# Kernel tuning notes

Measured on AMD Instinct MI355X. Metric: run time of the kernel, lower is better.

The kernel has to match this reference:

```python
import jax, jax.numpy as jnp
import numpy as np

H = 56; W = 56; WS = 7; SS = 3; NH = 12; DIM = 384; B = 32
N = WS * WS                      # 49 tokens per window
NW = (H // WS) * (W // WS)       # 64 windows per image
HID = 4 * DIM
EPS = 1e-5


def _rel_index():
    coords = np.stack(np.meshgrid(np.arange(WS), np.arange(WS), indexing='ij'))  # [2,ws,ws]
    cf = coords.reshape(2, -1)
    rel = (cf[:, :, None] - cf[:, None, :]).transpose(1, 2, 0)  # [N,N,2]
    rel[..., 0] += WS - 1
    rel[..., 1] += WS - 1
    rel[..., 0] *= 2 * WS - 1
    return rel.sum(-1).astype(np.int32)  # [N,N] in [0,169)


def _attn_mask():
    img = np.zeros((H, W), np.float32)
    cnt = 0
    sl = (slice(0, -WS), slice(-WS, -SS), slice(-SS, None))
    for h in sl:
        for w in sl:
            img[h, w] = cnt
            cnt += 1
    mw = img.reshape(H // WS, WS, W // WS, WS).transpose(0, 2, 1, 3).reshape(-1, N)  # [nW,N]
    am = mw[:, None, :] - mw[:, :, None]  # [nW,N,N]
    return np.where(am != 0, np.float32(-100.0), np.float32(0.0)).astype(np.float32)


def _ln(x, g, b):
    m = jnp.mean(x, axis=-1, keepdims=True)
    v = jnp.mean(jnp.square(x - m), axis=-1, keepdims=True)
    return (x - m) * jax.lax.rsqrt(v + EPS) * g + b


def setup_inputs() -> dict:
    key = jax.random.key(0)
    ks = jax.random.split(key, 8)
    s = 0.02
    return {
        'x': jax.random.normal(ks[0], (B, H * W, DIM), jnp.float32),
        'qkv_w': jax.random.normal(ks[1], (3 * DIM, DIM), jnp.float32) * s,
        'qkv_b': jnp.zeros((3 * DIM,), jnp.float32),
        'proj_w': jax.random.normal(ks[2], (DIM, DIM), jnp.float32) * s,
        'proj_b': jnp.zeros((DIM,), jnp.float32),
        'rpb_table': jax.random.normal(ks[3], ((2 * WS - 1) ** 2, NH), jnp.float32) * s,
        'ln1_g': jnp.ones((DIM,), jnp.float32),
        'ln1_b': jnp.zeros((DIM,), jnp.float32),
        'fc1_w': jax.random.normal(ks[4], (HID, DIM), jnp.float32) * s,
        'fc1_b': jnp.zeros((HID,), jnp.float32),
        'fc2_w': jax.random.normal(ks[5], (DIM, HID), jnp.float32) * s,
        'fc2_b': jnp.zeros((DIM,), jnp.float32),
        'ln2_g': jnp.ones((DIM,), jnp.float32),
        'ln2_b': jnp.zeros((DIM,), jnp.float32),
        'attn_mask': jnp.asarray(_attn_mask()),
        'rel_idx': jnp.asarray(_rel_index()),
    }


def reference(x, qkv_w, qkv_b, proj_w, proj_b, rpb_table, ln1_g, ln1_b,
              fc1_w, fc1_b, fc2_w, fc2_b, ln2_g, ln2_b, attn_mask, rel_idx):
    Bb, L, C = x.shape
    hd = C // NH
    scale = hd ** -0.5
    shortcut = x
    # cyclic shift
    xs = jnp.roll(x.reshape(Bb, H, W, C), (-SS, -SS), axis=(1, 2))
    # window partition -> [Bb*nW, N, C]
    xw = xs.reshape(Bb, H // WS, WS, W // WS, WS, C).transpose(0, 1, 3, 2, 4, 5).reshape(-1, N, C)
    # qkv
    qkv = (xw @ qkv_w.T + qkv_b).reshape(-1, N, 3, NH, hd).transpose(2, 0, 3, 1, 4)
    q, k, v = qkv[0] * scale, qkv[1], qkv[2]          # [Bb*nW, NH, N, hd]
    attn = jnp.einsum('whnd,whmd->whnm', q, k)        # [Bb*nW, NH, N, N]
    bias = rpb_table[rel_idx.reshape(-1)].reshape(N, N, NH).transpose(2, 0, 1)
    attn = attn + bias[None]
    # shifted-window mask
    attn = attn.reshape(Bb, NW, NH, N, N) + attn_mask[None, :, None]
    attn = jax.nn.softmax(attn.reshape(-1, NH, N, N), axis=-1)
    out = jnp.einsum('whnm,whmd->whnd', attn, v).transpose(0, 2, 1, 3).reshape(-1, N, C)
    out = out @ proj_w.T + proj_b
    # window reverse + roll back
    xs = out.reshape(Bb, H // WS, W // WS, WS, WS, C).transpose(0, 1, 3, 2, 4, 5).reshape(Bb, H, W, C)
    xs = jnp.roll(xs, (SS, SS), axis=(1, 2)).reshape(Bb, L, C)
    # post-norm residuals (as in source: shortcut + norm(attn_out); x += norm(ffn(x)))
    x1 = shortcut + _ln(xs, ln1_g, ln1_b)
    y = jax.nn.gelu(x1 @ fc1_w.T + fc1_b, approximate=False) @ fc2_w.T + fc2_b
    return x1 + _ln(y, ln2_g, ln2_b)
```

## Files before the change

kernel.cpp:

```cpp
#include <hip/hip_runtime.h>
#include <hip/hip_bf16.h>
#include <math.h>

typedef __hip_bfloat16 bf16;
typedef __bf16 bf16x8 __attribute__((ext_vector_type(8)));
typedef float f32x4 __attribute__((ext_vector_type(4)));

#define HH 56
#define WW 56
#define WSZ 7
#define SSH 3
#define NHEAD 12
#define CDIM 384
#define BBATCH 32
#define NTOK 49
#define NWIN 64
#define HIDD 1536
#define HD 32
#define NWTOT (BBATCH*NWIN)
#define MROWS (NWTOT*NTOK)
#define MHALF (MROWS/2)
#define LTOT (HH*WW)
#define EPSLN 1e-5f
#define QSCALE 0.17677669529663687f
#define NEGBIG -1e30f

enum { M_QK = 0, M_V = 1, M_FC1 = 2 };

__device__ __forceinline__ void gload16(const void* g, void* l) {
    __builtin_amdgcn_global_load_lds(
        (const __attribute__((address_space(1))) void*)g,
        (__attribute__((address_space(3))) void*)l, 16, 0, 0);
}

__device__ __forceinline__ unsigned short bfbits(float v) {
    bf16 b = __float2bfloat16(v);
    return *reinterpret_cast<unsigned short*>(&b);
}

__device__ __forceinline__ float fast_gelu(float v) {
    return v / (1.0f + __expf(-1.59576912f * v * fmaf(0.044715f, v * v, 1.0f)));
}

__device__ __forceinline__ int xcd_swz(int orig, int nwg) {
    const int q = nwg >> 3, r = nwg & 7;
    const int xcd = orig & 7, loc = orig >> 3;
    return (xcd < r ? xcd * (q + 1) : r * (q + 1) + (xcd - r) * q) + loc;
}

__global__ __launch_bounds__(256) void cvt_k(const float* __restrict__ src,
                                             bf16* __restrict__ dst, int n) {
    int i = blockIdx.x * 256 + threadIdx.x;
    if (i < n) dst[i] = __float2bfloat16(src[i]);
}

__global__ __launch_bounds__(256)
void tbl_k(const float* __restrict__ rpb, const int* __restrict__ relidx,
           const float* __restrict__ amask, float* __restrict__ tbl) {
    int idx = blockIdx.x * 256 + threadIdx.x;
    int m = idx & 63, n = (idx >> 6) & 63;
    int h = (idx >> 12) % NHEAD, wi = idx / (64 * 64 * NHEAD);
    float v;
    if (m >= NTOK) v = NEGBIG;
    else if (n >= NTOK) v = 0.f;
    else v = rpb[relidx[n * NTOK + m] * NHEAD + h] + amask[((long)wi * NTOK + n) * NTOK + m];
    tbl[idx] = v;
}

__global__ __launch_bounds__(256) void gather_k(const float* __restrict__ x,
                                                bf16* __restrict__ xw, int rbase) {
    int idx = blockIdx.x * 256 + threadIdx.x;
    int rr_l = idx / 96, c4 = (idx % 96) * 4;
    int rr = rbase + rr_l;
    int w = rr / 49, ti = rr % 49;
    int b = w >> 6, wi = w & 63;
    int hy = (wi >> 3) * 7 + ti / 7;
    int hx = (wi & 7) * 7 + ti % 7;
    int sh = hy + SSH; if (sh >= HH) sh -= HH;
    int sw = hx + SSH; if (sw >= WW) sw -= WW;
    float4 v = *(const float4*)&x[((long)b * LTOT + sh * WW + sw) * CDIM + c4];
    ushort4 u = { bfbits(v.x), bfbits(v.y), bfbits(v.z), bfbits(v.w) };
    *(ushort4*)&xw[(long)rr_l * CDIM + c4] = u;
}

template<int MODE, int KDIM, int NTN>
__global__ __launch_bounds__(256, 4)
void mgemm_k(const bf16* __restrict__ A, const bf16* __restrict__ Wt,
             const float* __restrict__ bias, void* __restrict__ Outp)
{
    constexpr bool SWAP = (MODE != M_V);
    __shared__ bf16 As[2][128 * 32];
    __shared__ bf16 Bs[2][128 * 32];
    const int tid = threadIdx.x;
    const int wid = tid >> 6, lane = tid & 63;

    const int gid = xcd_swz(blockIdx.x, gridDim.x);
    const int m0 = (gid / NTN) * 128;
    const int n0 = (gid % NTN) * 128;

    const int strow = lane >> 2, stseg = lane & 3;
    const int swseg = stseg ^ ((strow >> 1) & 3);
    const bf16* Ag = A + (long)(m0 + wid * 32 + strow) * KDIM + swseg * 8;
    const bf16* Wg = Wt + (long)(n0 + wid * 32 + strow) * KDIM + swseg * 8;

    const int wr = (wid >> 1) * 64, wc = (wid & 1) * 64;
    const int l15 = lane & 15, g4 = lane >> 4;
    const int sa = g4 ^ ((l15 >> 1) & 3);

    f32x4 acc[4][4] = {};

    auto STAGE = [&](int b, int t) {
#pragma unroll
        for (int i = 0; i < 2; ++i)
            gload16(Ag + (long)(i * 16) * KDIM + t * 32, &As[b][(wid * 32 + i * 16) * 32]);
#pragma unroll
        for (int i = 0; i < 2; ++i)
            gload16(Wg + (long)(i * 16) * KDIM + t * 32, &Bs[b][(wid * 32 + i * 16) * 32]);
    };

    const int nt = KDIM / 32;
    STAGE(0, 0);
    STAGE(1, 1);
    asm volatile("s_waitcnt vmcnt(4)" ::: "memory");
    __builtin_amdgcn_s_barrier();

    int buf = 0;
    for (int t = 0; t < nt; ++t) {
        bf16x8 af[4], bfr[4];
#pragma unroll
        for (int i = 0; i < 4; ++i) {
            af[i]  = *(const bf16x8*)&As[buf][(wr + i * 16 + l15) * 32 + sa * 8];
            bfr[i] = *(const bf16x8*)&Bs[buf][(wc + i * 16 + l15) * 32 + sa * 8];
        }
        __builtin_amdgcn_sched_barrier(0);
        asm volatile("s_waitcnt lgkmcnt(0)" ::: "memory");
        __builtin_amdgcn_sched_barrier(0);
        __builtin_amdgcn_s_barrier();
        if (t + 2 < nt) STAGE(buf, t + 2);
#pragma unroll
        for (int mi = 0; mi < 4; ++mi)
#pragma unroll
            for (int ni = 0; ni < 4; ++ni) {
                if (SWAP)
                    acc[ni][mi] = __builtin_amdgcn_mfma_f32_16x16x32_bf16(
                        bfr[ni], af[mi], acc[ni][mi], 0, 0, 0);
                else
                    acc[mi][ni] = __builtin_amdgcn_mfma_f32_16x16x32_bf16(
                        af[mi], bfr[ni], acc[mi][ni], 0, 0, 0);
            }
        if (t + 2 < nt) { asm volatile("s_waitcnt vmcnt(4)" ::: "memory"); }
        else            { asm volatile("s_waitcnt vmcnt(0)" ::: "memory"); }
        __builtin_amdgcn_s_barrier();
        buf ^= 1;
    }

    if (MODE == M_V) {
#pragma unroll
        for (int mi = 0; mi < 4; ++mi) {
            const int mb = m0 + wr + mi * 16 + g4 * 4;
            const int wv_ = mb / 49, ti0 = mb - wv_ * 49;
#pragma unroll
            for (int ni = 0; ni < 4; ++ni) {
                const int n = n0 + wc + ni * 16 + l15;
                const int h = n >> 5, d = n & 31;
                const float bn = bias[n];
                float v4[4];
#pragma unroll
                for (int j = 0; j < 4; ++j) v4[j] = acc[mi][ni][j] + bn;
                if (ti0 <= 45) {
                    ushort4 u = { bfbits(v4[0]), bfbits(v4[1]), bfbits(v4[2]), bfbits(v4[3]) };
                    *(ushort4*)&((bf16*)Outp)[(((long)wv_ * NHEAD + h) * HD + d) * 64 + ti0] = u;
                } else {
#pragma unroll
                    for (int j = 0; j < 4; ++j) {
                        const int m = mb + j;
                        const int w2 = m / 49, ti = m - w2 * 49;
                        ((bf16*)Outp)[(((long)w2 * NHEAD + h) * HD + d) * 64 + ti]
                            = __float2bfloat16(v4[j]);
                    }
                }
            }
        }
    } else {
        long rowbase[4];
        int wq_[4], ti_[4];
#pragma unroll
        for (int mi = 0; mi < 4; ++mi) {
            const int m = m0 + wr + mi * 16 + l15;
            if (MODE == M_QK) { wq_[mi] = m / 49; ti_[mi] = m - wq_[mi] * 49; }
            else              { rowbase[mi] = (long)m * HIDD; }
        }
#pragma unroll
        for (int ni = 0; ni < 4; ++ni) {
            const int nb = n0 + wc + ni * 16 + g4 * 4;
            const float4 bn = *(const float4*)&bias[nb];
            const float bb[4] = { bn.x, bn.y, bn.z, bn.w };
#pragma unroll
            for (int mi = 0; mi < 4; ++mi) {
                float v4[4];
#pragma unroll
                for (int j = 0; j < 4; ++j) v4[j] = acc[ni][mi][j] + bb[j];
                if (MODE == M_FC1) {
#pragma unroll
                    for (int j = 0; j < 4; ++j) v4[j] = fast_gelu(v4[j]);
                } else if (MODE == M_QK) {
                    if (nb < CDIM) {
#pragma unroll
                        for (int j = 0; j < 4; ++j) v4[j] *= QSCALE;
                    }
                }
                ushort4 u = { bfbits(v4[0]), bfbits(v4[1]), bfbits(v4[2]), bfbits(v4[3]) };
                if (MODE == M_QK) {
                    const int which = nb >= CDIM;
                    const int hb = (nb - which * CDIM) >> 5, d0 = nb & 31;
                    *(ushort4*)&((bf16*)Outp)[
                        ((((long)wq_[mi] * 2 + which) * NHEAD + hb) * NTOK + ti_[mi]) * HD + d0] = u;
                } else {
                    *(ushort4*)&((bf16*)Outp)[rowbase[mi] + nb] = u;
                }
            }
        }
    }
}

template<int KDIM, bool SCATTER>
__global__ __launch_bounds__(256, 2)
void gemm_ln_k(const bf16* __restrict__ A, const bf16* __restrict__ Wt,
               const float* __restrict__ bias, const bf16* __restrict__ resid,
               const float* __restrict__ lng, const float* __restrict__ lnb,
               float* __restrict__ outf, bf16* __restrict__ outb, int mbase)
{
    __shared__ bf16 As[2][64 * 32];
    __shared__ bf16 Bs[2][384 * 32];
    __shared__ float lnp[512];
    const int tid = threadIdx.x;
    const int wid = tid >> 6, lane = tid & 63;

    const int m0 = xcd_swz(blockIdx.x, gridDim.x) * 64;

    const int strow = tid >> 2, stseg = tid & 3;
    const int swr = stseg ^ ((strow >> 1) & 3);
    const bf16* Ag = A + (long)(m0 + strow) * KDIM + swr * 8;
    const bf16* Wg = Wt + (long)strow * KDIM + swr * 8;

    const int wc = wid * 96;
    const int l15 = lane & 15, g4 = lane >> 4;
    const int sa = g4 ^ ((l15 >> 1) & 3);

    f32x4 acc[6][4] = {};

    auto STAGE = [&](int b, int t) {
        gload16(Ag + t * 32, &As[b][strow * 32 + stseg * 8]);
#pragma unroll
        for (int i = 0; i < 6; ++i)
            gload16(Wg + (long)(i * 64) * KDIM + t * 32,
                    &Bs[b][(strow + i * 64) * 32 + stseg * 8]);
    };

    const int nt = KDIM / 32;
    STAGE(0, 0);
    STAGE(1, 1);
    asm volatile("s_waitcnt vmcnt(7)" ::: "memory");
    __builtin_amdgcn_s_barrier();

    int buf = 0;
    for (int t = 0; t < nt; ++t) {
        bf16x8 af[4], bfr[6];
#pragma unroll
        for (int i = 0; i < 4; ++i)
            af[i] = *(const bf16x8*)&As[buf][(i * 16 + l15) * 32 + sa * 8];
#pragma unroll
        for (int i = 0; i < 6; ++i)
            bfr[i] = *(const bf16x8*)&Bs[buf][(wc + i * 16 + l15) * 32 + sa * 8];
        __builtin_amdgcn_sched_barrier(0);
        asm volatile("s_waitcnt lgkmcnt(0)" ::: "memory");
        __builtin_amdgcn_sched_barrier(0);
        __builtin_amdgcn_s_barrier();
        if (t + 2 < nt) STAGE(buf, t + 2);
#pragma unroll
        for (int ni = 0; ni < 6; ++ni)
#pragma unroll
            for (int mi = 0; mi < 4; ++mi)
                acc[ni][mi] = __builtin_amdgcn_mfma_f32_16x16x32_bf16(
                    bfr[ni], af[mi], acc[ni][mi], 0, 0, 0);
        if (t + 2 < nt) { asm volatile("s_waitcnt vmcnt(7)" ::: "memory"); }
        else            { asm volatile("s_waitcnt vmcnt(0)" ::: "memory"); }
        __builtin_amdgcn_s_barrier();
        buf ^= 1;
    }

    float psum[4] = {}, psq[4] = {};
#pragma unroll
    for (int ni = 0; ni < 6; ++ni) {
        const int nb = wc + ni * 16 + g4 * 4;
        const float4 bn = *(const float4*)&bias[nb];
        const float bb[4] = { bn.x, bn.y, bn.z, bn.w };
#pragma unroll
        for (int mi = 0; mi < 4; ++mi)
#pragma unroll
            for (int j = 0; j < 4; ++j) {
                float v = acc[ni][mi][j] + bb[j];
                acc[ni][mi][j] = v;
                psum[mi] += v; psq[mi] += v * v;
            }
    }
#pragma unroll
    for (int mi = 0; mi < 4; ++mi) {
        psum[mi] += __shfl_xor(psum[mi], 16); psum[mi] += __shfl_xor(psum[mi], 32);
        psq[mi]  += __shfl_xor(psq[mi], 16);  psq[mi]  += __shfl_xor(psq[mi], 32);
    }
    if (g4 == 0) {
#pragma unroll
        for (int mi = 0; mi < 4; ++mi) {
            const int r = mi * 16 + l15;
            lnp[wid * 64 + r] = psum[mi];
            lnp[256 + wid * 64 + r] = psq[mi];
        }
    }
    __syncthreads();

#pragma unroll
    for (int mi = 0; mi < 4; ++mi) {
        const int r = mi * 16 + l15;
        const float s  = lnp[r] + lnp[64 + r] + lnp[128 + r] + lnp[192 + r];
        const float sq = lnp[256 + r] + lnp[320 + r] + lnp[384 + r] + lnp[448 + r];
        const float mean = s * (1.f / 384.f);
        const float rstd = rsqrtf(sq * (1.f / 384.f) - mean * mean + EPSLN);

        const long rl = m0 + r;
        long dst;
        if (SCATTER) {
            const int m = mbase + (int)rl;
            int w = m / 49, ti = m - w * 49;
            int b = w >> 6, wi = w & 63;
            int hy = (wi >> 3) * 7 + ti / 7;
            int hx = (wi & 7) * 7 + ti % 7;
            int dh = hy + SSH; if (dh >= HH) dh -= HH;
            int dw = hx + SSH; if (dw >= WW) dw -= WW;
            dst = (long)b * LTOT + dh * WW + dw - mbase;
        } else {
            dst = mbase + rl;
        }
#pragma unroll
        for (int ni = 0; ni < 6; ++ni) {
            const int c = wc + ni * 16 + g4 * 4;
            const float4 gv = *(const float4*)&lng[c];
            const float4 bv = *(const float4*)&lnb[c];
            ushort4 xv = *(const ushort4*)&resid[rl * CDIM + c];
            float x0 = __bfloat162float(*(bf16*)&xv.x);
            float x1 = __bfloat162float(*(bf16*)&xv.y);
            float x2 = __bfloat162float(*(bf16*)&xv.z);
            float x3 = __bfloat162float(*(bf16*)&xv.w);
            float r0 = x0 + (acc[ni][mi][0] - mean) * rstd * gv.x + bv.x;
            float r1 = x1 + (acc[ni][mi][1] - mean) * rstd * gv.y + bv.y;
            float r2 = x2 + (acc[ni][mi][2] - mean) * rstd * gv.z + bv.z;
            float r3 = x3 + (acc[ni][mi][3] - mean) * rstd * gv.w + bv.w;
            if (SCATTER) {
                ushort4 u = { bfbits(r0), bfbits(r1), bfbits(r2), bfbits(r3) };
                *(ushort4*)&outb[dst * CDIM + c] = u;
            } else {
                float4 o = { r0, r1, r2, r3 };
                *(float4*)&outf[dst * CDIM + c] = o;
            }
        }
    }
}

__global__ __launch_bounds__(256)
void mattn_k(const bf16* __restrict__ qk, const bf16* __restrict__ vT,
             const float* __restrict__ tbl, bf16* __restrict__ attn_out)
{
    __shared__ bf16 Plds[4][64 * 72];
    const int tid = threadIdx.x, wid = tid >> 6, lane = tid & 63;
    const int t = blockIdx.x * 4 + wid;
    const int w = t / NHEAD, h = t % NHEAD, wi = w & 63;
    const int l15 = lane & 15, g = lane >> 4;
    const bf16* qb = qk + ((long)(w * 2 + 0) * NHEAD + h) * (NTOK * HD);
    const bf16* kb = qk + ((long)(w * 2 + 1) * NHEAD + h) * (NTOK * HD);
    const bf16* vt = vT + ((long)w * NHEAD + h) * (HD * 64);
    const float* Tb = tbl + (long)(wi * NHEAD + h) * 64 * 64;
    char* Pw = (char*)&Plds[wid][0];

    bf16x8 kf[4], qf[4];
#pragma unroll
    for (int i = 0; i < 4; ++i) {
        kf[i] = *(const bf16x8*)&kb[(16 * i + l15) * HD + 8 * g];
        qf[i] = *(const bf16x8*)&qb[(16 * i + l15) * HD + 8 * g];
    }
    f32x4 s[4][4] = {};
#pragma unroll
    for (int mi = 0; mi < 4; ++mi)
#pragma unroll
        for (int ni = 0; ni < 4; ++ni)
            s[mi][ni] = __builtin_amdgcn_mfma_f32_16x16x32_bf16(
                kf[mi], qf[ni], s[mi][ni], 0, 0, 0);

#pragma unroll
    for (int ni = 0; ni < 4; ++ni) {
        const int n = 16 * ni + l15;
#pragma unroll
        for (int mi = 0; mi < 4; ++mi) {
            float4 tv = *(const float4*)&Tb[(long)n * 64 + 16 * mi + 4 * g];
            s[mi][ni][0] += tv.x; s[mi][ni][1] += tv.y;
            s[mi][ni][2] += tv.z; s[mi][ni][3] += tv.w;
        }
        float mx = NEGBIG;
#pragma unroll
        for (int mi = 0; mi < 4; ++mi)
#pragma unroll
            for (int j = 0; j < 4; ++j) mx = fmaxf(mx, s[mi][ni][j]);
        mx = fmaxf(mx, __shfl_xor(mx, 16));
        mx = fmaxf(mx, __shfl_xor(mx, 32));
        float sum = 0.f;
#pragma unroll
        for (int mi = 0; mi < 4; ++mi)
#pragma unroll
            for (int j = 0; j < 4; ++j) {
                float e = expf(s[mi][ni][j] - mx);
                s[mi][ni][j] = e; sum += e;
            }
        sum += __shfl_xor(sum, 16);
        sum += __shfl_xor(sum, 32);
        const float r = 1.0f / sum;
#pragma unroll
        for (int mi = 0; mi < 4; ++mi) {
            ushort4 u;
            u.x = bfbits(s[mi][ni][0] * r);
            u.y = bfbits(s[mi][ni][1] * r);
            u.z = bfbits(s[mi][ni][2] * r);
            u.w = bfbits(s[mi][ni][3] * r);
            *(ushort4*)(Pw + (long)n * 144 + (16 * mi + 4 * g) * 2) = u;
        }
    }

    f32x4 o[4][2] = {};
#pragma unroll
    for (int kk = 0; kk < 2; ++kk) {
        bf16x8 vf[2];
        vf[0] = *(const bf16x8*)&vt[(long)(l15) * 64 + 32 * kk + 8 * g];
        vf[1] = *(const bf16x8*)&vt[(long)(16 + l15) * 64 + 32 * kk + 8 * g];
#pragma unroll
        for (int rt = 0; rt < 4; ++rt) {
            bf16x8 pf = *(const bf16x8*)(Pw + (long)(16 * rt + l15) * 144 + (32 * kk + 8 * g) * 2);
            o[rt][0] = __builtin_amdgcn_mfma_f32_16x16x32_bf16(pf, vf[0], o[rt][0], 0, 0, 0);
            o[rt][1] = __builtin_amdgcn_mfma_f32_16x16x32_bf16(pf, vf[1], o[rt][1], 0, 0, 0);
        }
    }

#pragma unroll
    for (int rt = 0; rt < 4; ++rt)
#pragma unroll
        for (int dt = 0; dt < 2; ++dt)
#pragma unroll
            for (int j = 0; j < 4; ++j) {
                int n = 16 * rt + 4 * g + j;
                if (n < NTOK)
                    attn_out[((long)w * NTOK + n) * CDIM + h * HD + 16 * dt + l15]
                        = __float2bfloat16(o[rt][dt][j]);
            }
}

extern "C" void kernel_launch(void* const* d_in, const int* in_sizes, int n_in,
                              void* d_out, int out_size, void* d_ws, size_t ws_size,
                              hipStream_t stream)
{
    const float* x      = (const float*)d_in[0];
    const float* qkv_w  = (const float*)d_in[1];
    const float* qkv_b  = (const float*)d_in[2];
    const float* proj_w = (const float*)d_in[3];
    const float* proj_b = (const float*)d_in[4];
    const float* rpb    = (const float*)d_in[5];
    const float* ln1_g  = (const float*)d_in[6];
    const float* ln1_b  = (const float*)d_in[7];
    const float* fc1_w  = (const float*)d_in[8];
    const float* fc1_b  = (const float*)d_in[9];
    const float* fc2_w  = (const float*)d_in[10];
    const float* fc2_b  = (const float*)d_in[11];
    const float* ln2_g  = (const float*)d_in[12];
    const float* ln2_b  = (const float*)d_in[13];
    const float* amask  = (const float*)d_in[14];
    const int*   relidx = (const int*)d_in[15];
    float* out = (float*)d_out;
    char*  ws  = (char*)d_ws;

    bf16*  wq    = (bf16*) (ws + 0L);
    bf16*  wp    = (bf16*) (ws + 884736L);
    bf16*  w1    = (bf16*) (ws + 1179648L);
    bf16*  w2    = (bf16*) (ws + 2359296L);
    float* tbl   = (float*)(ws + 3538944L);
    bf16*  xw_h  = (bf16*) (ws + 16121856L);
    bf16*  qkb_h = (bf16*) (ws + 54657024L);
    bf16*  vT_h  = (bf16*) (ws + 131727360L);
    bf16*  att_h = (bf16*) (ws + 182059008L);
    bf16*  x1b_h = (bf16*) (ws + 220594176L);
    bf16*  H1_h  = (bf16*) (ws + 16121856L);

    dim3 b256(256);

    cvt_k<<<dim3((3*CDIM*CDIM + 255)/256), b256, 0, stream>>>(qkv_w, wq, 3*CDIM*CDIM);
    cvt_k<<<dim3((CDIM*CDIM + 255)/256), b256, 0, stream>>>(proj_w, wp, CDIM*CDIM);
    cvt_k<<<dim3((HIDD*CDIM + 255)/256), b256, 0, stream>>>(fc1_w, w1, HIDD*CDIM);
    cvt_k<<<dim3((CDIM*HIDD + 255)/256), b256, 0, stream>>>(fc2_w, w2, CDIM*HIDD);
    tbl_k<<<dim3(64*12*64*64/256), b256, 0, stream>>>(rpb, relidx, amask, tbl);

    for (int c = 0; c < 2; ++c) {
        const int mb = c * MHALF;
        gather_k<<<dim3(MHALF * 96 / 256), b256, 0, stream>>>(x, xw_h, mb);
        mgemm_k<M_QK, CDIM, 6><<<dim3((MHALF/128)*6), b256, 0, stream>>>(
            xw_h, wq, qkv_b, (void*)qkb_h);
        mgemm_k<M_V, CDIM, 3><<<dim3((MHALF/128)*3), b256, 0, stream>>>(
            xw_h, wq + (long)2*CDIM*CDIM, qkv_b + 2*CDIM, (void*)vT_h);
        mattn_k<<<dim3(1024 * NHEAD / 4), b256, 0, stream>>>(qkb_h, vT_h, tbl, att_h);
        gemm_ln_k<CDIM, true><<<dim3(MHALF/64), b256, 0, stream>>>(
            att_h, wp, proj_b, xw_h, ln1_g, ln1_b, nullptr, x1b_h, mb);
        mgemm_k<M_FC1, CDIM, 12><<<dim3((MHALF/128)*12), b256, 0, stream>>>(
            x1b_h, w1, fc1_b, (void*)H1_h);
        gemm_ln_k<HIDD, false><<<dim3(MHALF/64), b256, 0, stream>>>(
            H1_h, w2, fc2_b, x1b_h, ln2_g, ln2_b, out, nullptr, mb);
    }
}
```

Before: 888.4 us.

## Enlarge GEMM+LayerNorm tile to 128 rows with 512-thread blocks

The fused GEMM+LayerNorm kernels now process 128 rows per block using 8 waves arranged 2x4, instead of 64 rows with 4 waves. Each staged 384-column weight tile is therefore reused across twice as many rows, which halves weight traffic from global memory and L2 per output row. The per-thread load count in the staging pipeline and the LN partial-sum buffer are adjusted to match. The trade-off is larger LDS use per block, half as many blocks, and a launch bound of 4 blocks of 512 threads that may constrain registers.

```diff
diff --git a/kernel.cpp b/kernel.cpp
--- a/kernel.cpp
+++ b/kernel.cpp
@@ -224,26 +224,27 @@
 }
 
 template<int KDIM, bool SCATTER>
-__global__ __launch_bounds__(256, 2)
+__global__ __launch_bounds__(512, 4)
 void gemm_ln_k(const bf16* __restrict__ A, const bf16* __restrict__ Wt,
                const float* __restrict__ bias, const bf16* __restrict__ resid,
                const float* __restrict__ lng, const float* __restrict__ lnb,
                float* __restrict__ outf, bf16* __restrict__ outb, int mbase)
 {
-    __shared__ bf16 As[2][64 * 32];
+    __shared__ bf16 As[2][128 * 32];
     __shared__ bf16 Bs[2][384 * 32];
-    __shared__ float lnp[512];
+    __shared__ float lnp[1024];
     const int tid = threadIdx.x;
     const int wid = tid >> 6, lane = tid & 63;
 
-    const int m0 = xcd_swz(blockIdx.x, gridDim.x) * 64;
+    const int m0 = xcd_swz(blockIdx.x, gridDim.x) * 128;
 
     const int strow = tid >> 2, stseg = tid & 3;
-    const int swr = stseg ^ ((strow >> 1) & 3);
-    const bf16* Ag = A + (long)(m0 + strow) * KDIM + swr * 8;
-    const bf16* Wg = Wt + (long)strow * KDIM + swr * 8;
-
-    const int wc = wid * 96;
+    const int sws = stseg ^ ((strow >> 1) & 3);
+    const bf16* Ag = A + (long)(m0 + strow) * KDIM + sws * 8;
+    const bf16* Wg = Wt + (long)strow * KDIM + sws * 8;
+
+    const int wm = wid >> 2, wn = wid & 3;
+    const int wr = wm * 64, wc = wn * 96;
     const int l15 = lane & 15, g4 = lane >> 4;
     const int sa = g4 ^ ((l15 >> 1) & 3);
 
@@ -252,15 +253,15 @@
     auto STAGE = [&](int b, int t) {
         gload16(Ag + t * 32, &As[b][strow * 32 + stseg * 8]);
 #pragma unroll
-        for (int i = 0; i < 6; ++i)
-            gload16(Wg + (long)(i * 64) * KDIM + t * 32,
-                    &Bs[b][(strow + i * 64) * 32 + stseg * 8]);
+        for (int p = 0; p < 3; ++p)
+            gload16(Wg + (long)(p * 128) * KDIM + t * 32,
+                    &Bs[b][(p * 128 + strow) * 32 + stseg * 8]);
     };
 
     const int nt = KDIM / 32;
     STAGE(0, 0);
     STAGE(1, 1);
-    asm volatile("s_waitcnt vmcnt(7)" ::: "memory");
+    asm volatile("s_waitcnt vmcnt(4)" ::: "memory");
     __builtin_amdgcn_s_barrier();
 
     int buf = 0;
@@ -268,7 +269,7 @@
         bf16x8 af[4], bfr[6];
 #pragma unroll
         for (int i = 0; i < 4; ++i)
-            af[i] = *(const bf16x8*)&As[buf][(i * 16 + l15) * 32 + sa * 8];
+            af[i] = *(const bf16x8*)&As[buf][(wr + i * 16 + l15) * 32 + sa * 8];
 #pragma unroll
         for (int i = 0; i < 6; ++i)
             bfr[i] = *(const bf16x8*)&Bs[buf][(wc + i * 16 + l15) * 32 + sa * 8];
@@ -283,7 +284,7 @@
             for (int mi = 0; mi < 4; ++mi)
                 acc[ni][mi] = __builtin_amdgcn_mfma_f32_16x16x32_bf16(
                     bfr[ni], af[mi], acc[ni][mi], 0, 0, 0);
-        if (t + 2 < nt) { asm volatile("s_waitcnt vmcnt(7)" ::: "memory"); }
+        if (t + 2 < nt) { asm volatile("s_waitcnt vmcnt(4)" ::: "memory"); }
         else            { asm volatile("s_waitcnt vmcnt(0)" ::: "memory"); }
         __builtin_amdgcn_s_barrier();
         buf ^= 1;
@@ -312,18 +313,18 @@
     if (g4 == 0) {
 #pragma unroll
         for (int mi = 0; mi < 4; ++mi) {
-            const int r = mi * 16 + l15;
-            lnp[wid * 64 + r] = psum[mi];
-            lnp[256 + wid * 64 + r] = psq[mi];
+            const int r = wr + mi * 16 + l15;
+            lnp[wn * 128 + r] = psum[mi];
+            lnp[512 + wn * 128 + r] = psq[mi];
         }
     }
     __syncthreads();
 
 #pragma unroll
     for (int mi = 0; mi < 4; ++mi) {
-        const int r = mi * 16 + l15;
-        const float s  = lnp[r] + lnp[64 + r] + lnp[128 + r] + lnp[192 + r];
-        const float sq = lnp[256 + r] + lnp[320 + r] + lnp[384 + r] + lnp[448 + r];
+        const int r = wr + mi * 16 + l15;
+        const float s  = lnp[r] + lnp[128 + r] + lnp[256 + r] + lnp[384 + r];
+        const float sq = lnp[512 + r] + lnp[640 + r] + lnp[768 + r] + lnp[896 + r];
         const float mean = s * (1.f / 384.f);
         const float rstd = rsqrtf(sq * (1.f / 384.f) - mean * mean + EPSLN);
 
@@ -495,7 +496,7 @@
     bf16*  x1b_h = (bf16*) (ws + 220594176L);
     bf16*  H1_h  = (bf16*) (ws + 16121856L);
 
-    dim3 b256(256);
+    dim3 b256(256), b512(512);
 
     cvt_k<<<dim3((3*CDIM*CDIM + 255)/256), b256, 0, stream>>>(qkv_w, wq, 3*CDIM*CDIM);
     cvt_k<<<dim3((CDIM*CDIM + 255)/256), b256, 0, stream>>>(proj_w, wp, CDIM*CDIM);
@@ -511,11 +512,11 @@
         mgemm_k<M_V, CDIM, 3><<<dim3((MHALF/128)*3), b256, 0, stream>>>(
             xw_h, wq + (long)2*CDIM*CDIM, qkv_b + 2*CDIM, (void*)vT_h);
         mattn_k<<<dim3(1024 * NHEAD / 4), b256, 0, stream>>>(qkb_h, vT_h, tbl, att_h);
-        gemm_ln_k<CDIM, true><<<dim3(MHALF/64), b256, 0, stream>>>(
+        gemm_ln_k<CDIM, true><<<dim3(MHALF/128), b512, 0, stream>>>(
             att_h, wp, proj_b, xw_h, ln1_g, ln1_b, nullptr, x1b_h, mb);
         mgemm_k<M_FC1, CDIM, 12><<<dim3((MHALF/128)*12), b256, 0, stream>>>(
             x1b_h, w1, fc1_b, (void*)H1_h);
-        gemm_ln_k<HIDD, false><<<dim3(MHALF/64), b256, 0, stream>>>(
+        gemm_ln_k<HIDD, false><<<dim3(MHALF/128), b512, 0, stream>>>(
             H1_h, w2, fc2_b, x1b_h, ln2_g, ln2_b, out, nullptr, mb);
     }
 }
```

Result: slower. 1.794 ms (+101.9%).
